# Kernel optimization log

Measured on AMD Instinct MI355X. Metric: run time of the kernel, lower is better.

## Reference

```python
import jax, jax.numpy as jnp
import numpy as np

C = 6      # in_channel (forced by the module's own shape constraints)
MID = 3    # in_channel // 2
EPS = 1e-5


def setup_inputs() -> dict:
    key = jax.random.key(0)
    ks = jax.random.split(key, 16)
    B, N, NC, L = 2, 32768, 3, 2048
    w = lambda k, shape: jax.random.normal(k, shape, jnp.float32) * 0.2
    return {
        "x": jax.random.normal(ks[0], (B, C, N), jnp.float32),
        "curves": jax.random.normal(ks[1], (B, C, NC, L), jnp.float32),
        "Wa": w(ks[2], (MID, C)),    # conva   (Conv1d C->MID, k=1, no bias)
        "Wav": w(ks[3], (MID, C)),   # conva_v
        "Wb": w(ks[4], (MID, C)),    # convb
        "Wbv": w(ks[5], (MID, C)),   # convb_v
        "Wc": w(ks[6], (MID, C)),    # convc
        "Wd": w(ks[7], (C, 2 * MID)),  # convd Conv1d 2*MID -> C
        "bn_gamma": jnp.ones((C,), jnp.float32),
        "bn_beta": jnp.zeros((C,), jnp.float32),
        "Watt": w(ks[8], (C,)),      # line_conv_att Conv2d C->1, k=1
        "ln_gamma": jnp.ones((2 * MID,), jnp.float32),
        "ln_beta": jnp.zeros((2 * MID,), jnp.float32),
        "Wpl": w(ks[9], (MID, 3)),   # p_l Conv1d 3->MID (with bias)
        "bpl": w(ks[10], (MID,)),
        "Wpn": w(ks[11], (MID, 3)),  # p_n Conv1d 3->MID (with bias)
        "bpn": w(ks[12], (MID,)),
    }


def reference(x, curves, Wa, Wav, Wb, Wbv, Wc, Wd, bn_gamma, bn_beta,
              Watt, ln_gamma, ln_beta, Wpl, bpl, Wpn, bpn):
    # p, curve = curves  (tensor unpack along dim 0)
    p = curves[0]                                        # [C, 3, L]
    # p_l / p_n: Conv1d(3, MID) with p treated as batch=C, channels=3
    pl = jnp.einsum('bkl,mk->bml', p, Wpl) + bpl[None, :, None]   # [C, MID, L]
    p_l = pl.mean(axis=-1)                               # [C, MID]
    pn = jnp.einsum('bkl,mk->bml', p, Wpn) + bpn[None, :, None]   # [C, MID, L]
    p_n = pn.mean(axis=-2)                               # [C, L]

    # line attention over curves
    att = jnp.einsum('bcnl,c->bnl', curves, Watt)[:, None, :, :]  # [B,1,3,L]
    curver_inter = (curves * jax.nn.softmax(att, axis=-1)).sum(axis=-1)  # [B,C,3]
    curves_intra = (curves * jax.nn.softmax(att, axis=-2)).sum(axis=-2)  # [B,C,L]

    gi = curver_inter + p_l                              # [B,C,3] + [C,3(MID)]
    ga = curves_intra + p_n                              # [B,C,L] + [C,L]
    k_inter = jnp.einsum('bcn,mc->bmn', gi, Wa)          # [B,MID,3]
    v_inter = jnp.einsum('bcn,mc->bnm', gi, Wav)         # [B,3,MID]
    k_intra = jnp.einsum('bcl,mc->bml', ga, Wb)          # [B,MID,L]
    v_intra = jnp.einsum('bcl,mc->blm', ga, Wbv)         # [B,L,MID]

    q = jnp.einsum('bcn,mc->bnm', x, Wc)                 # [B,N,MID]
    scale = jnp.sqrt(jnp.float32(q.shape[-1]))           # sqrt(MID)

    att_inter = jax.nn.softmax(jnp.einsum('bnm,bmk->bnk', q, k_inter) / scale, axis=-1)
    feature_inter = jnp.einsum('bnk,bkm->bnm', att_inter, v_inter)   # [B,N,MID]
    att_intra = jax.nn.softmax(jnp.einsum('bnm,bml->bnl', q, k_intra) / scale, axis=-1)
    feature_intra = jnp.einsum('bnl,blm->bnm', att_intra, v_intra)   # [B,N,MID]

    cf = jnp.concatenate([feature_inter, feature_intra], axis=-1)    # [B,N,2*MID]
    mu = cf.mean(axis=-1, keepdims=True)
    var = ((cf - mu) ** 2).mean(axis=-1, keepdims=True)
    cf = (cf - mu) * jax.lax.rsqrt(var + EPS) * ln_gamma + ln_beta   # LayerNorm
    cf = jnp.swapaxes(cf, 1, 2)                                      # [B,2*MID,N]

    y = jnp.einsum('bcn,oc->bon', cf, Wd)                # Conv1d 2*MID -> C
    # BatchNorm1d (training-mode batch statistics over (B, N))
    bm = y.mean(axis=(0, 2), keepdims=True)
    bv = ((y - bm) ** 2).mean(axis=(0, 2), keepdims=True)
    y = (y - bm) * jax.lax.rsqrt(bv + EPS) * bn_gamma[None, :, None] + bn_beta[None, :, None]

    out = x + y
    return jnp.where(out >= 0, out, 0.2 * out)           # LeakyReLU(0.2)
```

## Files before the change

### kernel.cpp

```cpp
#include <hip/hip_runtime.h>
#include <math.h>

#define N_PTS 32768
#define LL    2048

#define KT_U      0
#define VT_U      8192
#define PART_OFF  16384
#define MS2_OFF   28672
#define W2_OFF    28768
#define CS2_OFF   29056
#define PBKM_OFF  29200

typedef __fp16 h2    __attribute__((ext_vector_type(2)));
typedef __fp16 f16x4 __attribute__((ext_vector_type(4)));
typedef float  f32x4 __attribute__((ext_vector_type(4)));

__device__ __forceinline__ unsigned h2_bits(h2 h){
  union { h2 h; unsigned u; } x; x.h = h; return x.u;
}
__device__ __forceinline__ float wave_reduce_sum(float v){
  #pragma unroll
  for (int off = 32; off; off >>= 1) v += __shfl_xor(v, off, 64);
  return v;
}
__device__ __forceinline__ float wave_reduce_max(float v){
  #pragma unroll
  for (int off = 32; off; off >>= 1) v = fmaxf(v, __shfl_xor(v, off, 64));
  return v;
}

__global__ __launch_bounds__(256)
void prep_kernel(const float* __restrict__ curves, const float* __restrict__ Watt,
                 const float* __restrict__ Wb,  const float* __restrict__ Wbv,
                 const float* __restrict__ Wpn, const float* __restrict__ bpn,
                 float* __restrict__ ws)
{
  const int blk = blockIdx.x, tid = threadIdx.x;
  const int lane = tid & 63, wid = tid >> 6;
  __shared__ float sred[4 * 13];
  __shared__ float msh;

  float watt[6];
  #pragma unroll
  for (int c = 0; c < 6; c++) watt[c] = Watt[c];

  if (blk < 48) {
    const int g = blk >> 3, s = blk & 7;
    const int b = g / 3, nc = g % 3;
    const int l = s * 256 + tid;
    const float* cb = curves + b * 18 * LL;

    float cv[6], av = 0.f;
    #pragma unroll
    for (int c = 0; c < 6; c++) {
      cv[c] = cb[(c * 3 + nc) * LL + l];
      av = fmaf(cv[c], watt[c], av);
    }
    float pm = wave_reduce_max(av);
    if (lane == 0) sred[wid] = pm;
    __syncthreads();
    if (tid == 0) msh = fmaxf(fmaxf(sred[0], sred[1]), fmaxf(sred[2], sred[3]));
    __syncthreads();
    const float m = msh;

    float vals[13];
    float e = __expf(av - m);
    vals[0] = e;
    #pragma unroll
    for (int c = 0; c < 6; c++) {
      vals[1 + c] = cv[c] * e;
      vals[7 + c] = cv[c];
    }
    __syncthreads();
    #pragma unroll
    for (int j = 0; j < 13; j++) vals[j] = wave_reduce_sum(vals[j]);
    if (lane == 0) { for (int j = 0; j < 13; j++) sred[wid * 13 + j] = vals[j]; }
    __syncthreads();
    if (tid == 0) {
      float t[13];
      for (int j = 0; j < 13; j++)
        t[j] = sred[j] + sred[13 + j] + sred[26 + j] + sred[39 + j];
      ws[MS2_OFF + (g * 8 + s) * 2]     = m;
      ws[MS2_OFF + (g * 8 + s) * 2 + 1] = t[0];
      for (int c = 0; c < 6; c++) ws[W2_OFF + (g * 8 + s) * 6 + c] = t[1 + c];
      if (b == 0)
        for (int c = 0; c < 6; c++) ws[CS2_OFF + (nc * 8 + s) * 6 + c] = t[7 + c];
    }
  } else {
    const int idx = (blk - 48) * 256 + tid;
    const int b = idx >> 10, pp = idx & 1023, l = pp * 2;
    const float* cb = curves + b * 18 * LL;

    float2 cv[6][3], pv[6][3];
    #pragma unroll
    for (int c = 0; c < 6; c++)
      #pragma unroll
      for (int nc = 0; nc < 3; nc++) {
        cv[c][nc] = *(const float2*)&cb[(c * 3 + nc) * LL + l];
        pv[c][nc] = *(const float2*)&curves[(c * 3 + nc) * LL + l];
      }
    float a[3][2];
    #pragma unroll
    for (int nc = 0; nc < 3; nc++) {
      float sx = 0.f, sy = 0.f;
      #pragma unroll
      for (int c = 0; c < 6; c++) {
        sx = fmaf(cv[c][nc].x, watt[c], sx);
        sy = fmaf(cv[c][nc].y, watt[c], sy);
      }
      a[nc][0] = sx; a[nc][1] = sy;
    }

    float wb_r[18], wbv_r[18];
    #pragma unroll
    for (int i = 0; i < 18; i++) { wb_r[i] = Wb[i]; wbv_r[i] = Wbv[i]; }
    const float wn0 = (Wpn[0] + Wpn[3] + Wpn[6]) * (1.f / 3.f);
    const float wn1 = (Wpn[1] + Wpn[4] + Wpn[7]) * (1.f / 3.f);
    const float wn2 = (Wpn[2] + Wpn[5] + Wpn[8]) * (1.f / 3.f);
    const float bnb = (bpn[0] + bpn[1] + bpn[2]) * (1.f / 3.f);

    float kk[2][3], vv[2][3], km[3] = {0.f, 0.f, 0.f};
    #pragma unroll
    for (int e = 0; e < 2; e++) {
      float a0 = a[0][e], a1 = a[1][e], a2 = a[2][e];
      float mm = fmaxf(fmaxf(a0, a1), a2);
      float e0 = __expf(a0 - mm), e1 = __expf(a1 - mm), e2 = __expf(a2 - mm);
      float r = 1.f / (e0 + e1 + e2);
      float ga[6];
      #pragma unroll
      for (int c = 0; c < 6; c++) {
        float c0 = e ? cv[c][0].y : cv[c][0].x;
        float c1 = e ? cv[c][1].y : cv[c][1].x;
        float c2 = e ? cv[c][2].y : cv[c][2].x;
        float p0 = e ? pv[c][0].y : pv[c][0].x;
        float p1 = e ? pv[c][1].y : pv[c][1].x;
        float p2 = e ? pv[c][2].y : pv[c][2].x;
        float intra = (c0 * e0 + c1 * e1 + c2 * e2) * r;
        float pn = p0 * wn0 + p1 * wn1 + p2 * wn2 + bnb;
        ga[c] = intra + pn;
      }
      float k0 = 0, k1 = 0, k2 = 0, v0 = 0, v1 = 0, v2 = 0;
      #pragma unroll
      for (int c = 0; c < 6; c++) {
        k0 += wb_r[c] * ga[c];  k1 += wb_r[6 + c] * ga[c];  k2 += wb_r[12 + c] * ga[c];
        v0 += wbv_r[c] * ga[c]; v1 += wbv_r[6 + c] * ga[c]; v2 += wbv_r[12 + c] * ga[c];
      }
      kk[e][0] = k0; kk[e][1] = k1; kk[e][2] = k2;
      vv[e][0] = v0; vv[e][1] = v1; vv[e][2] = v2;
      km[0] = fmaxf(km[0], fabsf(k0));
      km[1] = fmaxf(km[1], fabsf(k1));
      km[2] = fmaxf(km[2], fabsf(k2));
    }

    unsigned* ktg = (unsigned*)ws + KT_U + b * 4096;
    #pragma unroll
    for (int e = 0; e < 2; e++) {
      const int k = l + e;
      const int idxk = (k >> 5) * 64 + (k & 15) * 4 + (((k >> 4) & 1) << 1);
      ktg[idxk]     = h2_bits(__builtin_amdgcn_cvt_pkrtz(kk[e][0], kk[e][1]));
      ktg[idxk + 1] = h2_bits(__builtin_amdgcn_cvt_pkrtz(kk[e][2], 0.f));
    }
    {
      unsigned* vtg = (unsigned*)ws + VT_U + b * 4096;
      const int cp = pp >> 4, c2 = (pp >> 3) & 1, p = (2 * pp) & 15;
      const int base = cp * 64 + (p >> 2) * 4 + c2 * 2 + ((p >> 1) & 1);
      vtg[base]      = h2_bits(__builtin_amdgcn_cvt_pkrtz(vv[0][0], vv[1][0]));
      vtg[base + 16] = h2_bits(__builtin_amdgcn_cvt_pkrtz(vv[0][1], vv[1][1]));
      vtg[base + 32] = h2_bits(__builtin_amdgcn_cvt_pkrtz(vv[0][2], vv[1][2]));
      vtg[base + 48] = h2_bits(__builtin_amdgcn_cvt_pkrtz(1.f, 1.f));
    }

    #pragma unroll
    for (int j = 0; j < 3; j++) km[j] = wave_reduce_max(km[j]);
    if (lane == 0) { for (int j = 0; j < 3; j++) sred[wid * 3 + j] = km[j]; }
    __syncthreads();
    if (tid == 0) {
      for (int j = 0; j < 3; j++)
        ws[PBKM_OFF + (blk - 48) * 3 + j] =
          fmaxf(fmaxf(sred[j], sred[3 + j]), fmaxf(sred[6 + j], sred[9 + j]));
    }
  }
}

__global__ __launch_bounds__(512, 8)
void attn_kernel(const float* __restrict__ x,  const float* __restrict__ Wc,
                 const float* __restrict__ Wd, const float* __restrict__ lng,
                 const float* __restrict__ lnb,
                 const float* __restrict__ Wa, const float* __restrict__ Wav,
                 const float* __restrict__ Wpl, const float* __restrict__ bpl,
                 float* __restrict__ ws, float* __restrict__ yout)
{
  __shared__ __align__(16) unsigned kt[4104];
  __shared__ __align__(16) unsigned vt[4104];
  __shared__ float4 cross[4][4][16];
  __shared__ float gis[18], kis[9], vis[9];
  const int tid  = threadIdx.x, blk = blockIdx.x;
  const int lane = tid & 63, w = tid >> 6;
  const int col  = lane & 15, hi4 = lane >> 4;
  const int rp   = w >> 2, kq = w & 3;
  const int rbase = blk * 64;
  const int b    = rbase >> 15;
  const int nb   = rbase & (N_PTS - 1);

  {
    const uint4* ktg = (const uint4*)((const unsigned*)ws + KT_U + b * 4096);
    const uint4* vtg = (const uint4*)((const unsigned*)ws + VT_U + b * 4096);
    uint4* kt4 = (uint4*)kt;
    uint4* vt4 = (uint4*)vt;
    for (int i = tid; i < 1024; i += 512) { kt4[i] = ktg[i]; vt4[i] = vtg[i]; }
    if (tid < 8) { kt[4096 + tid] = 0; vt[4096 + tid] = 0; }
  }
  if (tid < 18) {
    const int c = tid / 3, m = tid % 3;
    const int g = b * 3 + m;
    float mx = -1e30f;
    #pragma unroll
    for (int s = 0; s < 8; s++) mx = fmaxf(mx, ws[MS2_OFF + (g * 8 + s) * 2]);
    float sum = 0.f, Wc_ = 0.f;
    #pragma unroll
    for (int s = 0; s < 8; s++) {
      float e = __expf(ws[MS2_OFF + (g * 8 + s) * 2] - mx);
      sum += ws[MS2_OFF + (g * 8 + s) * 2 + 1] * e;
      Wc_ += ws[W2_OFF + (g * 8 + s) * 6 + c] * e;
    }
    float pl_ = bpl[m];
    #pragma unroll
    for (int k = 0; k < 3; k++) {
      float cs = 0.f;
      #pragma unroll
      for (int s = 0; s < 8; s++) cs += ws[CS2_OFF + (k * 8 + s) * 6 + c];
      pl_ = fmaf(Wpl[m * 3 + k], cs * (1.f / LL), pl_);
    }
    gis[c * 3 + m] = Wc_ / sum + pl_;
  }
  __syncthreads();
  if (tid < 9) {
    int m = tid / 3, k = tid % 3;
    float s1 = 0.f, s2 = 0.f;
    #pragma unroll
    for (int c = 0; c < 6; c++) {
      float g = gis[c * 3 + k];
      s1 = fmaf(Wa [m * 6 + c], g, s1);
      s2 = fmaf(Wav[m * 6 + c], g, s2);
    }
    kis[m * 3 + k] = s1; vis[k * 3 + m] = s2;
  }

  float km0 = 0.f, km1 = 0.f, km2 = 0.f;
  #pragma unroll
  for (int s = 0; s < 4; s++) {
    const float* pk = ws + PBKM_OFF + (b * 4 + s) * 3;
    km0 = fmaxf(km0, pk[0]); km1 = fmaxf(km1, pk[1]); km2 = fmaxf(km2, pk[2]);
  }

  const int nA = nb + rp * 32 + col;
  const float* xb = x + (size_t)b * 6 * N_PTS;
  float q0A = 0, q1A = 0, q2A = 0, q0B = 0, q1B = 0, q2B = 0;
  #pragma unroll
  for (int c = 0; c < 6; c++) {
    float xvA = xb[c * N_PTS + nA], xvB = xb[c * N_PTS + nA + 16];
    q0A = fmaf(xvA, Wc[c], q0A); q1A = fmaf(xvA, Wc[6 + c], q1A); q2A = fmaf(xvA, Wc[12 + c], q2A);
    q0B = fmaf(xvB, Wc[c], q0B); q1B = fmaf(xvB, Wc[6 + c], q1B); q2B = fmaf(xvB, Wc[12 + c], q2B);
  }
  const float KS = 1.4426950408889634f * 0.57735026918962576f;
  q0A *= KS; q1A *= KS; q2A *= KS; q0B *= KS; q1B *= KS; q2B *= KS;
  const float MpA = fabsf(q0A) * km0 + fabsf(q1A) * km1 + fabsf(q2A) * km2;
  const float MpB = fabsf(q0B) * km0 + fabsf(q1B) * km1 + fabsf(q2B) * km2;

  union U2 { uint2 u; f16x4 h; };
  union U4 { uint4 q; f16x4 h[2]; };
  U2 qbA, qbB;
  qbA.u.x = qbA.u.y = qbB.u.x = qbB.u.y = 0;
  if (hi4 == 0) {
    qbA.u.x = h2_bits(__builtin_amdgcn_cvt_pkrtz(q0A, q1A));
    qbA.u.y = h2_bits(__builtin_amdgcn_cvt_pkrtz(q2A, 0.f));
    qbB.u.x = h2_bits(__builtin_amdgcn_cvt_pkrtz(q0B, q1B));
    qbB.u.y = h2_bits(__builtin_amdgcn_cvt_pkrtz(q2B, 0.f));
  }
  f32x4 cbA = { -MpA, -MpA, -MpA, -MpA };
  f32x4 cbB = { -MpB, -MpB, -MpB, -MpB };
  f32x4 aA = {0,0,0,0}, aB = {0,0,0,0};

  unsigned ki_ = (hi4 == 0) ? (unsigned)(kq * 1024 + col * 4) : 4096u;
  const unsigned kd = (hi4 == 0) ? 64u : 0u;
  unsigned vi_ = (col < 4) ? (unsigned)(kq * 1024 + col * 16 + hi4 * 4) : 4096u;
  const unsigned vd = (col < 4) ? 64u : 0u;

  __syncthreads();

  for (int i = 0; i < 16; i++) {
    U4 K, V;
    K.q = *(const uint4*)&kt[ki_];
    V.q = *(const uint4*)&vt[vi_];
    ki_ += kd; vi_ += vd;

    f32x4 s0A = __builtin_amdgcn_mfma_f32_16x16x16f16(K.h[0], qbA.h, cbA, 0, 0, 0);
    f32x4 s0B = __builtin_amdgcn_mfma_f32_16x16x16f16(K.h[0], qbB.h, cbB, 0, 0, 0);
    f32x4 s1A = __builtin_amdgcn_mfma_f32_16x16x16f16(K.h[1], qbA.h, cbA, 0, 0, 0);
    f32x4 s1B = __builtin_amdgcn_mfma_f32_16x16x16f16(K.h[1], qbB.h, cbB, 0, 0, 0);

    U2 PA, PB;
    {
      float e0 = __builtin_amdgcn_exp2f(s0A[0]);
      float e1 = __builtin_amdgcn_exp2f(s0A[1]);
      float e2 = __builtin_amdgcn_exp2f(s0A[2]);
      float e3 = __builtin_amdgcn_exp2f(s0A[3]);
      float f0 = __builtin_amdgcn_exp2f(s0B[0]);
      float f1 = __builtin_amdgcn_exp2f(s0B[1]);
      float f2 = __builtin_amdgcn_exp2f(s0B[2]);
      float f3 = __builtin_amdgcn_exp2f(s0B[3]);
      PA.u.x = h2_bits(__builtin_amdgcn_cvt_pkrtz(e0, e1));
      PA.u.y = h2_bits(__builtin_amdgcn_cvt_pkrtz(e2, e3));
      PB.u.x = h2_bits(__builtin_amdgcn_cvt_pkrtz(f0, f1));
      PB.u.y = h2_bits(__builtin_amdgcn_cvt_pkrtz(f2, f3));
    }
    aA = __builtin_amdgcn_mfma_f32_16x16x16f16(V.h[0], PA.h, aA, 0, 0, 0);
    aB = __builtin_amdgcn_mfma_f32_16x16x16f16(V.h[0], PB.h, aB, 0, 0, 0);
    {
      float e0 = __builtin_amdgcn_exp2f(s1A[0]);
      float e1 = __builtin_amdgcn_exp2f(s1A[1]);
      float e2 = __builtin_amdgcn_exp2f(s1A[2]);
      float e3 = __builtin_amdgcn_exp2f(s1A[3]);
      float f0 = __builtin_amdgcn_exp2f(s1B[0]);
      float f1 = __builtin_amdgcn_exp2f(s1B[1]);
      float f2 = __builtin_amdgcn_exp2f(s1B[2]);
      float f3 = __builtin_amdgcn_exp2f(s1B[3]);
      PA.u.x = h2_bits(__builtin_amdgcn_cvt_pkrtz(e0, e1));
      PA.u.y = h2_bits(__builtin_amdgcn_cvt_pkrtz(e2, e3));
      PB.u.x = h2_bits(__builtin_amdgcn_cvt_pkrtz(f0, f1));
      PB.u.y = h2_bits(__builtin_amdgcn_cvt_pkrtz(f2, f3));
    }
    aA = __builtin_amdgcn_mfma_f32_16x16x16f16(V.h[1], PA.h, aA, 0, 0, 0);
    aB = __builtin_amdgcn_mfma_f32_16x16x16f16(V.h[1], PB.h, aB, 0, 0, 0);
  }

  if (hi4 == 0) {
    cross[rp * 2][kq][col]     = make_float4(aA[0], aA[1], aA[2], aA[3]);
    cross[rp * 2 + 1][kq][col] = make_float4(aB[0], aB[1], aB[2], aB[3]);
  }
  __syncthreads();

  if (tid < 64) {
    const int rt = tid >> 4, ri = tid & 15;
    const int n = nb + tid;
    float4 c0 = cross[rt][0][ri], c1 = cross[rt][1][ri];
    float4 c2 = cross[rt][2][ri], c3 = cross[rt][3][ri];
    float w0 = c0.x + c1.x + c2.x + c3.x;
    float w1 = c0.y + c1.y + c2.y + c3.y;
    float w2 = c0.z + c1.z + c2.z + c3.z;
    float dd = c0.w + c1.w + c2.w + c3.w;

    float a0 = 0, a1 = 0, a2 = 0;
    #pragma unroll
    for (int c = 0; c < 6; c++) {
      float xv = xb[c * N_PTS + n];
      a0 = fmaf(xv, Wc[c], a0); a1 = fmaf(xv, Wc[6 + c], a1); a2 = fmaf(xv, Wc[12 + c], a2);
    }
    a0 *= KS; a1 *= KS; a2 *= KS;

    float sk0 = a0 * kis[0] + a1 * kis[3] + a2 * kis[6];
    float sk1 = a0 * kis[1] + a1 * kis[4] + a2 * kis[7];
    float sk2 = a0 * kis[2] + a1 * kis[5] + a2 * kis[8];
    float mm  = fmaxf(fmaxf(sk0, sk1), sk2);
    float e0 = __builtin_amdgcn_exp2f(sk0 - mm);
    float e1 = __builtin_amdgcn_exp2f(sk1 - mm);
    float e2 = __builtin_amdgcn_exp2f(sk2 - mm);
    float rs = 1.f / (e0 + e1 + e2);
    float fi0 = (e0 * vis[0] + e1 * vis[3] + e2 * vis[6]) * rs;
    float fi1 = (e0 * vis[1] + e1 * vis[4] + e2 * vis[7]) * rs;
    float fi2 = (e0 * vis[2] + e1 * vis[5] + e2 * vis[8]) * rs;
    float rinv = 1.f / dd;
    float cf[6] = { fi0, fi1, fi2, w0 * rinv, w1 * rinv, w2 * rinv };

    float mu = (cf[0] + cf[1] + cf[2] + cf[3] + cf[4] + cf[5]) * (1.f / 6.f);
    float var = 0.f;
    #pragma unroll
    for (int i = 0; i < 6; i++) { float t = cf[i] - mu; var += t * t; }
    var *= (1.f / 6.f);
    float rn = rsqrtf(var + 1e-5f);
    float cfn[6];
    #pragma unroll
    for (int i = 0; i < 6; i++) cfn[i] = (cf[i] - mu) * rn * lng[i] + lnb[i];

    float v12[12];
    #pragma unroll
    for (int o = 0; o < 6; o++) {
      float s = 0.f;
      #pragma unroll
      for (int c = 0; c < 6; c++) s += Wd[o * 6 + c] * cfn[c];
      yout[(size_t)b * (6 * N_PTS) + o * N_PTS + n] = s;
      v12[o] = s; v12[6 + o] = s * s;
    }
    #pragma unroll
    for (int j = 0; j < 12; j++) v12[j] = wave_reduce_sum(v12[j]);
    if (tid == 0) {
      #pragma unroll
      for (int j = 0; j < 12; j++) ws[PART_OFF + j * 1024 + blk] = v12[j];
    }
  }
}

__global__ __launch_bounds__(256)
void final_kernel(const float* __restrict__ x,
                  const float* __restrict__ bng, const float* __restrict__ bnbt,
                  const float* __restrict__ ws, float* __restrict__ out)
{
  __shared__ float cp[48];
  __shared__ float sc_s[6], sh_s[6];
  const int tid = threadIdx.x, blk = blockIdx.x;
  const int lane = tid & 63, wid = tid >> 6;
  const float* part = ws + PART_OFF;

  float v[12];
  #pragma unroll
  for (int j = 0; j < 12; j++) {
    float4 p = *(const float4*)&part[j * 1024 + tid * 4];
    v[j] = p.x + p.y + p.z + p.w;
  }
  #pragma unroll
  for (int j = 0; j < 12; j++) v[j] = wave_reduce_sum(v[j]);
  if (lane == 0) { for (int j = 0; j < 12; j++) cp[wid * 12 + j] = v[j]; }
  __syncthreads();
  if (tid < 6) {
    const float inv = 1.f / 65536.f;
    float s1 = cp[tid] + cp[12 + tid] + cp[24 + tid] + cp[36 + tid];
    float s2 = cp[6 + tid] + cp[18 + tid] + cp[30 + tid] + cp[42 + tid];
    float mean = s1 * inv;
    float varr = s2 * inv - mean * mean;
    float sc = bng[tid] * rsqrtf(varr + 1e-5f);
    sc_s[tid] = sc;
    sh_s[tid] = bnbt[tid] - mean * sc;
  }
  __syncthreads();

  const int base = blk * 1024 + tid * 4;
  const int ch = (base >> 15) % 6;
  const float sc = sc_s[ch], sh = sh_s[ch];
  float4 o = *(float4*)&out[base];
  float4 xx = *(const float4*)&x[base];
  float r[4] = { o.x * sc + sh + xx.x, o.y * sc + sh + xx.y,
                 o.z * sc + sh + xx.z, o.w * sc + sh + xx.w };
  #pragma unroll
  for (int j = 0; j < 4; j++) r[j] = r[j] >= 0.f ? r[j] : 0.2f * r[j];
  *(float4*)&out[base] = make_float4(r[0], r[1], r[2], r[3]);
}

extern "C" void kernel_launch(void* const* d_in, const int* in_sizes, int n_in,
                              void* d_out, int out_size, void* d_ws, size_t ws_size,
                              hipStream_t stream)
{
  const float* x      = (const float*)d_in[0];
  const float* curves = (const float*)d_in[1];
  const float* Wa     = (const float*)d_in[2];
  const float* Wav    = (const float*)d_in[3];
  const float* Wb     = (const float*)d_in[4];
  const float* Wbv    = (const float*)d_in[5];
  const float* Wc     = (const float*)d_in[6];
  const float* Wd     = (const float*)d_in[7];
  const float* bng    = (const float*)d_in[8];
  const float* bnbt   = (const float*)d_in[9];
  const float* Watt   = (const float*)d_in[10];
  const float* lng    = (const float*)d_in[11];
  const float* lnbt   = (const float*)d_in[12];
  const float* Wpl    = (const float*)d_in[13];
  const float* bpl    = (const float*)d_in[14];
  const float* Wpn    = (const float*)d_in[15];
  const float* bpn    = (const float*)d_in[16];
  float* out = (float*)d_out;
  float* ws  = (float*)d_ws;

  prep_kernel<<<56, 256, 0, stream>>>(curves, Watt, Wb, Wbv, Wpn, bpn, ws);
  attn_kernel<<<1024, 512, 0, stream>>>(x, Wc, Wd, lng, lnbt,
                                        Wa, Wav, Wpl, bpl, ws, out);
  final_kernel<<<384, 256, 0, stream>>>(x, bng, bnbt, ws, out);
}
```

Measured before the change: 33.48 us.

## Fuse BatchNorm finalize into attention kernel via cooperative grid sync

Merges the final BatchNorm/residual/LeakyReLU kernel into the attention kernel using a cooperative launch with a grid-wide sync. The intermediate y values and x stay in registers instead of taking a round trip through global memory, and one kernel launch is removed. To fit all blocks in a single co-resident grid, each block now covers 128 points with 512 blocks, and each wave handles half of the key range instead of a quarter. The grid sync adds a global barrier and reduces the parallelism split over keys.

```diff
diff --git a/kernel.cpp b/kernel.cpp
--- a/kernel.cpp
+++ b/kernel.cpp
@@ -1,5 +1,8 @@
 #include <hip/hip_runtime.h>
+#include <hip/hip_cooperative_groups.h>
 #include <math.h>
+
+namespace cg = cooperative_groups;
 
 #define N_PTS 32768
 #define LL    2048
@@ -189,19 +192,21 @@
                  const float* __restrict__ lnb,
                  const float* __restrict__ Wa, const float* __restrict__ Wav,
                  const float* __restrict__ Wpl, const float* __restrict__ bpl,
-                 float* __restrict__ ws, float* __restrict__ yout)
+                 const float* __restrict__ bng, const float* __restrict__ bnbt,
+                 float* __restrict__ ws, float* __restrict__ out)
 {
   __shared__ __align__(16) unsigned kt[4104];
   __shared__ __align__(16) unsigned vt[4104];
-  __shared__ float4 cross[4][4][16];
+  __shared__ float4 cross[8][2][16];
   __shared__ float gis[18], kis[9], vis[9];
+  __shared__ float cpb[96];
+  __shared__ float sc_s[6], sh_s[6];
   const int tid  = threadIdx.x, blk = blockIdx.x;
   const int lane = tid & 63, w = tid >> 6;
   const int col  = lane & 15, hi4 = lane >> 4;
-  const int rp   = w >> 2, kq = w & 3;
-  const int rbase = blk * 64;
-  const int b    = rbase >> 15;
-  const int nb   = rbase & (N_PTS - 1);
+  const int rp   = w >> 1, kh = w & 1;
+  const int b    = blk >> 8;
+  const int nb   = (blk & 255) * 128;
 
   {
     const uint4* ktg = (const uint4*)((const unsigned*)ws + KT_U + b * 4096);
@@ -282,14 +287,14 @@
   f32x4 cbB = { -MpB, -MpB, -MpB, -MpB };
   f32x4 aA = {0,0,0,0}, aB = {0,0,0,0};
 
-  unsigned ki_ = (hi4 == 0) ? (unsigned)(kq * 1024 + col * 4) : 4096u;
+  unsigned ki_ = (hi4 == 0) ? (unsigned)(kh * 2048 + col * 4) : 4096u;
   const unsigned kd = (hi4 == 0) ? 64u : 0u;
-  unsigned vi_ = (col < 4) ? (unsigned)(kq * 1024 + col * 16 + hi4 * 4) : 4096u;
+  unsigned vi_ = (col < 4) ? (unsigned)(kh * 2048 + col * 16 + hi4 * 4) : 4096u;
   const unsigned vd = (col < 4) ? 64u : 0u;
 
   __syncthreads();
 
-  for (int i = 0; i < 16; i++) {
+  for (int i = 0; i < 32; i++) {
     U4 K, V;
     K.q = *(const uint4*)&kt[ki_];
     V.q = *(const uint4*)&vt[vi_];
@@ -336,26 +341,23 @@
   }
 
   if (hi4 == 0) {
-    cross[rp * 2][kq][col]     = make_float4(aA[0], aA[1], aA[2], aA[3]);
-    cross[rp * 2 + 1][kq][col] = make_float4(aB[0], aB[1], aB[2], aB[3]);
+    cross[rp * 2][kh][col]     = make_float4(aA[0], aA[1], aA[2], aA[3]);
+    cross[rp * 2 + 1][kh][col] = make_float4(aB[0], aB[1], aB[2], aB[3]);
   }
   __syncthreads();
 
-  if (tid < 64) {
+  float yv[6], xr[6];
+  if (tid < 128) {
     const int rt = tid >> 4, ri = tid & 15;
     const int n = nb + tid;
     float4 c0 = cross[rt][0][ri], c1 = cross[rt][1][ri];
-    float4 c2 = cross[rt][2][ri], c3 = cross[rt][3][ri];
-    float w0 = c0.x + c1.x + c2.x + c3.x;
-    float w1 = c0.y + c1.y + c2.y + c3.y;
-    float w2 = c0.z + c1.z + c2.z + c3.z;
-    float dd = c0.w + c1.w + c2.w + c3.w;
+    float w0 = c0.x + c1.x, w1 = c0.y + c1.y, w2 = c0.z + c1.z, dd = c0.w + c1.w;
 
     float a0 = 0, a1 = 0, a2 = 0;
     #pragma unroll
     for (int c = 0; c < 6; c++) {
-      float xv = xb[c * N_PTS + n];
-      a0 = fmaf(xv, Wc[c], a0); a1 = fmaf(xv, Wc[6 + c], a1); a2 = fmaf(xv, Wc[12 + c], a2);
+      xr[c] = xb[c * N_PTS + n];
+      a0 = fmaf(xr[c], Wc[c], a0); a1 = fmaf(xr[c], Wc[6 + c], a1); a2 = fmaf(xr[c], Wc[12 + c], a2);
     }
     a0 *= KS; a1 *= KS; a2 *= KS;
 
@@ -389,61 +391,55 @@
       float s = 0.f;
       #pragma unroll
       for (int c = 0; c < 6; c++) s += Wd[o * 6 + c] * cfn[c];
-      yout[(size_t)b * (6 * N_PTS) + o * N_PTS + n] = s;
+      yv[o] = s;
       v12[o] = s; v12[6 + o] = s * s;
     }
     #pragma unroll
     for (int j = 0; j < 12; j++) v12[j] = wave_reduce_sum(v12[j]);
-    if (tid == 0) {
-      #pragma unroll
-      for (int j = 0; j < 12; j++) ws[PART_OFF + j * 1024 + blk] = v12[j];
-    }
-  }
-}
-
-__global__ __launch_bounds__(256)
-void final_kernel(const float* __restrict__ x,
-                  const float* __restrict__ bng, const float* __restrict__ bnbt,
-                  const float* __restrict__ ws, float* __restrict__ out)
-{
-  __shared__ float cp[48];
-  __shared__ float sc_s[6], sh_s[6];
-  const int tid = threadIdx.x, blk = blockIdx.x;
-  const int lane = tid & 63, wid = tid >> 6;
-  const float* part = ws + PART_OFF;
-
-  float v[12];
-  #pragma unroll
-  for (int j = 0; j < 12; j++) {
-    float4 p = *(const float4*)&part[j * 1024 + tid * 4];
-    v[j] = p.x + p.y + p.z + p.w;
-  }
-  #pragma unroll
-  for (int j = 0; j < 12; j++) v[j] = wave_reduce_sum(v[j]);
-  if (lane == 0) { for (int j = 0; j < 12; j++) cp[wid * 12 + j] = v[j]; }
+    if (lane == 0) { for (int j = 0; j < 12; j++) cpb[(tid >> 6) * 12 + j] = v12[j]; }
+  }
   __syncthreads();
-  if (tid < 6) {
-    const float inv = 1.f / 65536.f;
-    float s1 = cp[tid] + cp[12 + tid] + cp[24 + tid] + cp[36 + tid];
-    float s2 = cp[6 + tid] + cp[18 + tid] + cp[30 + tid] + cp[42 + tid];
-    float mean = s1 * inv;
-    float varr = s2 * inv - mean * mean;
-    float sc = bng[tid] * rsqrtf(varr + 1e-5f);
-    sc_s[tid] = sc;
-    sh_s[tid] = bnbt[tid] - mean * sc;
-  }
-  __syncthreads();
-
-  const int base = blk * 1024 + tid * 4;
-  const int ch = (base >> 15) % 6;
-  const float sc = sc_s[ch], sh = sh_s[ch];
-  float4 o = *(float4*)&out[base];
-  float4 xx = *(const float4*)&x[base];
-  float r[4] = { o.x * sc + sh + xx.x, o.y * sc + sh + xx.y,
-                 o.z * sc + sh + xx.z, o.w * sc + sh + xx.w };
-  #pragma unroll
-  for (int j = 0; j < 4; j++) r[j] = r[j] >= 0.f ? r[j] : 0.2f * r[j];
-  *(float4*)&out[base] = make_float4(r[0], r[1], r[2], r[3]);
+  if (tid == 0) {
+    #pragma unroll
+    for (int j = 0; j < 12; j++)
+      ws[PART_OFF + j * 512 + blk] = cpb[j] + cpb[12 + j];
+  }
+
+  cg::this_grid().sync();
+
+  {
+    float v[12];
+    #pragma unroll
+    for (int j = 0; j < 12; j++) v[j] = ws[PART_OFF + j * 512 + tid];
+    #pragma unroll
+    for (int j = 0; j < 12; j++) v[j] = wave_reduce_sum(v[j]);
+    if (lane == 0) { for (int j = 0; j < 12; j++) cpb[w * 12 + j] = v[j]; }
+    __syncthreads();
+    if (tid < 6) {
+      const float inv = 1.f / 65536.f;
+      float s1 = 0.f, s2 = 0.f;
+      #pragma unroll
+      for (int ww = 0; ww < 8; ww++) {
+        s1 += cpb[ww * 12 + tid];
+        s2 += cpb[ww * 12 + 6 + tid];
+      }
+      float mean = s1 * inv;
+      float varr = s2 * inv - mean * mean;
+      float sc = bng[tid] * rsqrtf(varr + 1e-5f);
+      sc_s[tid] = sc;
+      sh_s[tid] = bnbt[tid] - mean * sc;
+    }
+    __syncthreads();
+  }
+
+  if (tid < 128) {
+    const int n = nb + tid;
+    #pragma unroll
+    for (int o = 0; o < 6; o++) {
+      float v = yv[o] * sc_s[o] + sh_s[o] + xr[o];
+      out[(size_t)b * (6 * N_PTS) + o * N_PTS + n] = v >= 0.f ? v : 0.2f * v;
+    }
+  }
 }
 
 extern "C" void kernel_launch(void* const* d_in, const int* in_sizes, int n_in,
@@ -471,7 +467,12 @@
   float* ws  = (float*)d_ws;
 
   prep_kernel<<<56, 256, 0, stream>>>(curves, Watt, Wb, Wbv, Wpn, bpn, ws);
-  attn_kernel<<<1024, 512, 0, stream>>>(x, Wc, Wd, lng, lnbt,
-                                        Wa, Wav, Wpl, bpl, ws, out);
-  final_kernel<<<384, 256, 0, stream>>>(x, bng, bnbt, ws, out);
-}
+
+  void* args[] = {
+    (void*)&x, (void*)&Wc, (void*)&Wd, (void*)&lng, (void*)&lnbt,
+    (void*)&Wa, (void*)&Wav, (void*)&Wpl, (void*)&bpl,
+    (void*)&bng, (void*)&bnbt, (void*)&ws, (void*)&out
+  };
+  hipLaunchCooperativeKernel((const void*)attn_kernel,
+                             dim3(512), dim3(512), args, 0, stream);
+}
```

New measurement: 79.82 us. +138.4%, slower.
